# Kernel tuning notes

Measured on AMD Instinct MI355X. Metric: run time of the kernel, lower is better.

Reference implementation:

```python
import jax, jax.numpy as jnp
import numpy as np

N_NODES = 100000
N_EDGES = 800000
D_IN = 128
D_HID = 128
D_OUT = 128
NUM_GRAPHS = 64


def gcn_conv(x, src, dst, W, b, n_nodes):
    """PyG GCNConv: h = D^{-1/2} (A + I) D^{-1/2} (x W) + b, with self-loops included in src/dst."""
    h = x @ W  # [N, d_out]
    deg = jax.ops.segment_sum(jnp.ones_like(dst, dtype=h.dtype), dst, num_segments=n_nodes)
    dinv = jnp.where(deg > 0, jax.lax.rsqrt(deg), 0.0)
    norm = dinv[src] * dinv[dst]  # [E]
    out = jax.ops.segment_sum(h[src] * norm[:, None], dst, num_segments=n_nodes)
    return out + b


def setup_inputs() -> dict:
    key = jax.random.key(0)
    ks = jax.random.split(key, 10)
    x = jax.random.normal(ks[0], (N_NODES, D_IN), dtype=jnp.float32)
    edge_index = jax.random.randint(ks[1], (2, N_EDGES), 0, N_NODES, dtype=jnp.int64)
    batch = jnp.sort(jax.random.randint(ks[2], (N_NODES,), 0, NUM_GRAPHS, dtype=jnp.int64))
    s1 = 1.0 / np.sqrt(D_IN)
    s2 = 1.0 / np.sqrt(D_HID)
    W1 = jax.random.uniform(ks[3], (D_IN, D_HID), jnp.float32, -s1, s1)
    b1 = jnp.zeros((D_HID,), jnp.float32)
    W2 = jax.random.uniform(ks[4], (D_HID, D_HID), jnp.float32, -s2, s2)
    b2 = jnp.zeros((D_HID,), jnp.float32)
    Wfc = jax.random.uniform(ks[5], (D_HID, D_OUT), jnp.float32, -s2, s2)
    bfc = jax.random.uniform(ks[6], (D_OUT,), jnp.float32, -s2, s2)
    return {"x": x, "edge_index": edge_index, "batch": batch,
            "W1": W1, "b1": b1, "W2": W2, "b2": b2, "Wfc": Wfc, "bfc": bfc}


def reference(x, edge_index, batch, W1, b1, W2, b2, Wfc, bfc):
    n = x.shape[0]
    loop = jnp.arange(n, dtype=edge_index.dtype)
    src = jnp.concatenate([edge_index[0], loop])
    dst = jnp.concatenate([edge_index[1], loop])
    h = jax.nn.relu(gcn_conv(x, src, dst, W1, b1, n))
    h = jax.nn.relu(gcn_conv(h, src, dst, W2, b2, n))
    # global_mean_pool over graph ids
    sums = jax.ops.segment_sum(h, batch, num_segments=NUM_GRAPHS)
    cnts = jax.ops.segment_sum(jnp.ones((n,), h.dtype), batch, num_segments=NUM_GRAPHS)
    pooled = sums / jnp.maximum(cnts, 1.0)[:, None]
    return pooled @ Wfc + bfc
```

## Files before the change

kernel.cpp:

```cpp
#include <hip/hip_runtime.h>
#include <hip/hip_bf16.h>

#define N_NODES 100000
#define N_EDGES 800000
#define D 128
#define NG 64
#define SCAN_NB ((N_NODES + 255) / 256)
#define NTILES ((N_NODES + 63) / 64)

typedef __attribute__((ext_vector_type(8))) short short8;
typedef __attribute__((ext_vector_type(4))) float f32x4;
typedef __attribute__((ext_vector_type(2))) float f32x2;

static __device__ __forceinline__ unsigned short f2bf(float f) {
    unsigned u = __float_as_uint(f);
    unsigned r = (u + 0x7FFF + ((u >> 16) & 1)) >> 16;
    return (unsigned short)r;
}
static __device__ __forceinline__ float bf2f(unsigned short b) {
    return __uint_as_float((unsigned)b << 16);
}
static __device__ __forceinline__ unsigned char f2fp8(float v) {
    int p = __builtin_amdgcn_cvt_pk_fp8_f32(v, v, 0, false);
    return (unsigned char)(p & 0xFF);
}


__global__ void hist_kernel(const int* __restrict__ dst, int* __restrict__ deg) {
    int e = blockIdx.x * blockDim.x + threadIdx.x;
    if (e < N_EDGES) atomicAdd(&deg[dst[e]], 1);
}

__global__ __launch_bounds__(256) void scan1_kernel(const int* __restrict__ deg,
                                                    int* __restrict__ rs,
                                                    int* __restrict__ bsum,
                                                    float* __restrict__ dinv) {
    __shared__ int wsum[4];
    int i = blockIdx.x * 256 + threadIdx.x;
    int lane = threadIdx.x & 63;
    int wid = threadIdx.x >> 6;
    int v = (i < N_NODES) ? deg[i] : 0;
    if (i < N_NODES) dinv[i] = rsqrtf((float)v + 1.0f);
    int x = v;
    #pragma unroll
    for (int off = 1; off < 64; off <<= 1) {
        int y = __shfl_up(x, off);
        if (lane >= off) x += y;
    }
    if (lane == 63) wsum[wid] = x;
    __syncthreads();
    int add = 0;
    #pragma unroll
    for (int w = 0; w < 3; ++w) if (w < wid) add += wsum[w];
    int incl = x + add;
    if (i < N_NODES) rs[i] = incl - v;
    if (threadIdx.x == 255) bsum[blockIdx.x] = incl;
}

__global__ __launch_bounds__(512) void scan2_kernel(int* __restrict__ bsum) {
    __shared__ int s[512];
    int t = threadIdx.x;
    int v = (t < SCAN_NB) ? bsum[t] : 0;
    s[t] = v;
    __syncthreads();
    for (int off = 1; off < 512; off <<= 1) {
        int y = (t >= off) ? s[t - off] : 0;
        __syncthreads();
        s[t] += y;
        __syncthreads();
    }
    if (t < SCAN_NB) bsum[t] = s[t] - v;
}

__global__ void scan3_kernel(int* __restrict__ rs, const int* __restrict__ bsum) {
    int i = blockIdx.x * blockDim.x + threadIdx.x;
    if (i < N_NODES) rs[i] += bsum[i >> 8];
    if (i == 0) rs[N_NODES] = N_EDGES;
}

__global__ void fill_kernel(const int* __restrict__ src, const int* __restrict__ dst,
                            const float* __restrict__ dinv, const int* __restrict__ rs,
                            int* __restrict__ cursor, int2* __restrict__ pairs) {
    int e = blockIdx.x * blockDim.x + threadIdx.x;
    if (e < N_EDGES) {
        int d = dst[e];
        int s = src[e];
        int p = rs[d] + atomicAdd(&cursor[d], 1);
        pairs[p] = make_int2(s, __float_as_int(dinv[s] * dinv[d]));
    }
}


__global__ void bounds_kernel(const int* __restrict__ batch, int* __restrict__ start) {
    int g = threadIdx.x;
    if (g > NG) return;
    if (g == NG) { start[NG] = N_NODES; return; }
    int lo = 0, hi = N_NODES;
    while (lo < hi) {
        int mid = (lo + hi) >> 1;
        if (batch[mid] < g) lo = mid + 1; else hi = mid;
    }
    start[g] = lo;
}


template <bool IN_F32>
__global__ __launch_bounds__(512) void xw_mfma_kernel(const void* __restrict__ Xin,
                                                      const float* __restrict__ W,
                                                      unsigned char* __restrict__ Hq) {
    __shared__ __align__(16) unsigned short bt_hi[128 * 128];
    __shared__ __align__(16) unsigned short bt_lo[128 * 128];
    __shared__ __align__(16) unsigned short atile[64 * 128];

    const int t = threadIdx.x;
    const int lane = t & 63;
    const int wid = t >> 6;

    #pragma unroll 4
    for (int i = 0; i < 32; ++i) {
        int idx = t + i * 512;
        int k = idx >> 7;
        int n = idx & 127;
        float w = W[idx];
        unsigned short hi = f2bf(w);
        unsigned short lo = f2bf(w - bf2f(hi));
        int byte = (n * 256 + k * 2) ^ ((n & 7) << 4);
        *(unsigned short*)((char*)bt_hi + byte) = hi;
        *(unsigned short*)((char*)bt_lo + byte) = lo;
    }

    const int mrow = (wid >> 1) * 16;
    const int ncol = (wid & 1) * 64;
    const int ar = mrow + (lane & 15);
    const int ak = (lane >> 4) * 8;

    for (int tile = blockIdx.x; tile < NTILES; tile += gridDim.x) {
        const int node0 = tile * 64;
        __syncthreads();

        #pragma unroll
        for (int p = 0; p < 2; ++p) {
            int j = t + p * 512;
            int row = j >> 4;
            int c8 = (j & 15) * 8;
            int node = node0 + row;
            short8 v = 0;
            if (IN_F32) {
                const float* X = (const float*)Xin;
                if (node < N_NODES) {
                    const float* xr = &X[(size_t)node * 128 + c8];
                    float4 a = *(const float4*)xr;
                    float4 b = *(const float4*)(xr + 4);
                    v[0] = (short)f2bf(a.x); v[1] = (short)f2bf(a.y);
                    v[2] = (short)f2bf(a.z); v[3] = (short)f2bf(a.w);
                    v[4] = (short)f2bf(b.x); v[5] = (short)f2bf(b.y);
                    v[6] = (short)f2bf(b.z); v[7] = (short)f2bf(b.w);
                }
            } else {
                const unsigned short* X = (const unsigned short*)Xin;
                if (node < N_NODES) v = *(const short8*)&X[(size_t)node * 128 + c8];
            }
            int byte = (row * 256 + c8 * 2) ^ ((row & 7) << 4);
            *(short8*)((char*)atile + byte) = v;
        }
        __syncthreads();

        f32x4 acc[4];
        #pragma unroll
        for (int nt = 0; nt < 4; ++nt) acc[nt] = 0.f;

        #pragma unroll
        for (int kc = 0; kc < 128; kc += 32) {
            short8 a = *(const short8*)((const char*)atile +
                        ((ar * 256 + (kc + ak) * 2) ^ ((ar & 7) << 4)));
            #pragma unroll
            for (int nt = 0; nt < 4; ++nt) {
                int col = ncol + nt * 16 + (lane & 15);
                int boff = (col * 256 + (kc + ak) * 2) ^ ((col & 7) << 4);
                short8 bh = *(const short8*)((const char*)bt_hi + boff);
                acc[nt] = __builtin_amdgcn_mfma_f32_16x16x32_bf16(a, bh, acc[nt], 0, 0, 0);
                short8 bl = *(const short8*)((const char*)bt_lo + boff);
                acc[nt] = __builtin_amdgcn_mfma_f32_16x16x32_bf16(a, bl, acc[nt], 0, 0, 0);
            }
        }

        #pragma unroll
        for (int nt = 0; nt < 4; ++nt) {
            #pragma unroll
            for (int r = 0; r < 4; ++r) {
                int node = node0 + mrow + (lane >> 4) * 4 + r;
                if (node < N_NODES)
                    Hq[(size_t)node * 128 + ncol + nt * 16 + (lane & 15)] = f2fp8(acc[nt][r]);
            }
        }
    }
}


#define ACC8(HV, W)                                                        \
    {                                                                      \
        f32x2 _h0 = __builtin_amdgcn_cvt_pk_f32_fp8((int)(HV).x, false);   \
        f32x2 _h1 = __builtin_amdgcn_cvt_pk_f32_fp8((int)(HV).x, true);    \
        f32x2 _h2 = __builtin_amdgcn_cvt_pk_f32_fp8((int)(HV).y, false);   \
        f32x2 _h3 = __builtin_amdgcn_cvt_pk_f32_fp8((int)(HV).y, true);    \
        acc[0] = fmaf(_h0[0], (W), acc[0]); acc[1] = fmaf(_h0[1], (W), acc[1]); \
        acc[2] = fmaf(_h1[0], (W), acc[2]); acc[3] = fmaf(_h1[1], (W), acc[3]); \
        acc[4] = fmaf(_h2[0], (W), acc[4]); acc[5] = fmaf(_h2[1], (W), acc[5]); \
        acc[6] = fmaf(_h3[0], (W), acc[6]); acc[7] = fmaf(_h3[1], (W), acc[7]); \
    }

__global__ __launch_bounds__(256) void gather_kernel(const unsigned char* __restrict__ Hq,
                                                     const int* __restrict__ rs,
                                                     const int2* __restrict__ pairs,
                                                     const float* __restrict__ dinv,
                                                     const float* __restrict__ bias,
                                                     unsigned short* __restrict__ out) {
    int node = blockIdx.x * 4 + (threadIdx.x >> 6);
    if (node >= N_NODES) return;
    const int lane = threadIdx.x & 63;
    const int g = lane >> 4;
    const int fl = lane & 15;

    int beg = rs[node];
    int end = rs[node + 1];
    int deg = end - beg;

    float di = dinv[node];
    float wself = (g == 0) ? di * di : 0.f;

    float acc[8];
    {
        uint2 sv = *(const uint2*)&Hq[(size_t)node * 128 + fl * 8];
        f32x2 a0 = __builtin_amdgcn_cvt_pk_f32_fp8((int)sv.x, false);
        f32x2 a1 = __builtin_amdgcn_cvt_pk_f32_fp8((int)sv.x, true);
        f32x2 a2 = __builtin_amdgcn_cvt_pk_f32_fp8((int)sv.y, false);
        f32x2 a3 = __builtin_amdgcn_cvt_pk_f32_fp8((int)sv.y, true);
        acc[0] = a0[0] * wself; acc[1] = a0[1] * wself;
        acc[2] = a1[0] * wself; acc[3] = a1[1] * wself;
        acc[4] = a2[0] * wself; acc[5] = a2[1] * wself;
        acc[6] = a3[0] * wself; acc[7] = a3[1] * wself;
    }

    if (deg > 0) {
        int2 pall = pairs[beg + min(lane, deg - 1)];
        int niter = (deg + 3) >> 2;

        const int j0 = g, j1 = g + 4, j2 = g + 8, j3 = g + 12;
        int s0 = __shfl(pall.x, j0), s1 = __shfl(pall.x, j1);
        int s2 = __shfl(pall.x, j2), s3 = __shfl(pall.x, j3);
        float w0 = (j0 < deg) ? __int_as_float(__shfl(pall.y, j0)) : 0.f;
        float w1 = (j1 < deg) ? __int_as_float(__shfl(pall.y, j1)) : 0.f;
        float w2 = (j2 < deg) ? __int_as_float(__shfl(pall.y, j2)) : 0.f;
        float w3 = (j3 < deg) ? __int_as_float(__shfl(pall.y, j3)) : 0.f;

        uint2 h0 = make_uint2(0u, 0u), h1 = h0, h2 = h0, h3 = h0;
        h0 = *(const uint2*)&Hq[(size_t)s0 * 128 + fl * 8];
        if (niter > 1) h1 = *(const uint2*)&Hq[(size_t)s1 * 128 + fl * 8];
        if (niter > 2) h2 = *(const uint2*)&Hq[(size_t)s2 * 128 + fl * 8];
        if (niter > 3) h3 = *(const uint2*)&Hq[(size_t)s3 * 128 + fl * 8];

        ACC8(h0, w0);
        ACC8(h1, w1);
        ACC8(h2, w2);
        ACC8(h3, w3);

        if (deg > 16) {
            for (int j = 16 + g; j < deg; j += 4) {
                int2 p = pairs[beg + j];
                float w = __int_as_float(p.y);
                uint2 hv = *(const uint2*)&Hq[(size_t)p.x * 128 + fl * 8];
                ACC8(hv, w);
            }
        }
    }

    #pragma unroll
    for (int mask = 16; mask <= 32; mask <<= 1) {
        #pragma unroll
        for (int j = 0; j < 8; ++j) acc[j] += __shfl_xor(acc[j], mask);
    }

    if (g == 0) {
        float4 bb0 = *(const float4*)&bias[fl * 8];
        float4 bb1 = *(const float4*)&bias[fl * 8 + 4];
        short8 o;
        o[0] = (short)f2bf(fmaxf(acc[0] + bb0.x, 0.f));
        o[1] = (short)f2bf(fmaxf(acc[1] + bb0.y, 0.f));
        o[2] = (short)f2bf(fmaxf(acc[2] + bb0.z, 0.f));
        o[3] = (short)f2bf(fmaxf(acc[3] + bb0.w, 0.f));
        o[4] = (short)f2bf(fmaxf(acc[4] + bb1.x, 0.f));
        o[5] = (short)f2bf(fmaxf(acc[5] + bb1.y, 0.f));
        o[6] = (short)f2bf(fmaxf(acc[6] + bb1.z, 0.f));
        o[7] = (short)f2bf(fmaxf(acc[7] + bb1.w, 0.f));
        *(short8*)&out[(size_t)node * 128 + fl * 8] = o;
    }
}


__global__ __launch_bounds__(256) void pool_kernel(const unsigned short* __restrict__ G,
                                                   const int* __restrict__ start,
                                                   float* __restrict__ sums) {
    __shared__ float red[16][132];
    int g = blockIdx.x >> 4;
    int s = blockIdx.x & 15;
    int n0 = start[g], n1 = start[g + 1];
    int slot = threadIdx.x & 15;
    int nl = threadIdx.x >> 4;

    float acc[8];
    #pragma unroll
    for (int j = 0; j < 8; ++j) acc[j] = 0.f;

    for (int node = n0 + s * 16 + nl; node < n1; node += 256) {
        short8 v = *(const short8*)&G[(size_t)node * 128 + slot * 8];
        #pragma unroll
        for (int j = 0; j < 8; ++j) acc[j] += bf2f((unsigned short)v[j]);
    }

    #pragma unroll
    for (int j = 0; j < 8; ++j) red[nl][slot * 8 + j] = acc[j];
    __syncthreads();
    #pragma unroll
    for (int off = 8; off > 0; off >>= 1) {
        if (nl < off) {
            #pragma unroll
            for (int j = 0; j < 8; ++j)
                red[nl][slot * 8 + j] += red[nl + off][slot * 8 + j];
        }
        __syncthreads();
    }
    if (nl == 0) {
        #pragma unroll
        for (int j = 0; j < 8; ++j)
            unsafeAtomicAdd(&sums[g * D + slot * 8 + j], red[0][slot * 8 + j]);
    }
}


__global__ void fc_kernel(const float* __restrict__ sums, const int* __restrict__ start,
                          const float* __restrict__ Wfc, const float* __restrict__ bfc,
                          float* __restrict__ out) {
    __shared__ __align__(16) float ps[D];
    int g = blockIdx.x;
    int f = threadIdx.x;
    float c = (float)max(start[g + 1] - start[g], 1);
    ps[f] = sums[g * D + f] / c;
    __syncthreads();
    float acc = bfc[f];
    #pragma unroll
    for (int k = 0; k < D; k += 4) {
        float4 pv = *(const float4*)&ps[k];
        acc += pv.x * Wfc[k * D + f] + pv.y * Wfc[(k + 1) * D + f] +
               pv.z * Wfc[(k + 2) * D + f] + pv.w * Wfc[(k + 3) * D + f];
    }
    out[g * D + f] = acc;
}

extern "C" void kernel_launch(void* const* d_in, const int* in_sizes, int n_in,
                              void* d_out, int out_size, void* d_ws, size_t ws_size,
                              hipStream_t stream) {
    const float* x   = (const float*)d_in[0];
    const int* ei    = (const int*)d_in[1];
    const int* batch = (const int*)d_in[2];
    const float* W1  = (const float*)d_in[3];
    const float* b1  = (const float*)d_in[4];
    const float* W2  = (const float*)d_in[5];
    const float* b2  = (const float*)d_in[6];
    const float* Wfc = (const float*)d_in[7];
    const float* bfc = (const float*)d_in[8];
    float* out = (float*)d_out;

    const int* src = ei;
    const int* dst = ei + N_EDGES;

    unsigned char* Hq    = (unsigned char*)d_ws;
    unsigned short* G    = (unsigned short*)(Hq + (size_t)N_NODES * D);
    int2* pairs          = (int2*)(G + (size_t)N_NODES * D);
    float* dinv          = (float*)(pairs + N_EDGES);
    int*   deg           = (int*)(dinv + N_NODES);
    int*   cursor        = deg + N_NODES;
    int*   rs            = cursor + N_NODES;
    int*   bsum          = rs + N_NODES + 4;
    int*   start         = bsum + 512;
    float* sums          = (float*)(start + NG + 8);

    hipMemsetAsync(deg, 0, 2 * N_NODES * sizeof(int), stream);
    hipMemsetAsync(sums, 0, NG * D * sizeof(float), stream);

    hist_kernel<<<(N_EDGES + 255) / 256, 256, 0, stream>>>(dst, deg);
    scan1_kernel<<<SCAN_NB, 256, 0, stream>>>(deg, rs, bsum, dinv);
    scan2_kernel<<<1, 512, 0, stream>>>(bsum);
    scan3_kernel<<<SCAN_NB, 256, 0, stream>>>(rs, bsum);
    fill_kernel<<<(N_EDGES + 255) / 256, 256, 0, stream>>>(src, dst, dinv, rs, cursor, pairs);
    bounds_kernel<<<1, 128, 0, stream>>>(batch, start);

    xw_mfma_kernel<true><<<512, 512, 0, stream>>>(x, W1, Hq);
    gather_kernel<<<(N_NODES + 3) / 4, 256, 0, stream>>>(Hq, rs, pairs, dinv, b1, G);

    xw_mfma_kernel<false><<<512, 512, 0, stream>>>(G, W2, Hq);
    gather_kernel<<<(N_NODES + 3) / 4, 256, 0, stream>>>(Hq, rs, pairs, dinv, b2, G);

    pool_kernel<<<NG * 16, 256, 0, stream>>>(G, start, sums);
    fc_kernel<<<NG, 128, 0, stream>>>(sums, start, Wfc, bfc, out);
}
```

Baseline: 305.7 us.

## Fold symmetric normalization into XW output and drop per-edge weights

The per-edge weight dinv[s]*dinv[d] is factored: H rows are pre-scaled by dinv[src] in the matmul epilogue and the aggregated sum is scaled by dinv[dst] in the gather epilogue. Edge storage shrinks from int2 pairs to plain source ids, and the fill kernel drops the dinv reads. The CSR row-start array now doubles as the cursor through a shifted scan, which removes one array and its memset. Padded lanes point at a zeroed sentinel row instead of using zero weights. This lowers memory traffic in the fill and gather stages, at the cost of rounding dinv-scaled values to fp8.

```diff
diff --git a/kernel.cpp b/kernel.cpp
--- a/kernel.cpp
+++ b/kernel.cpp
@@ -53,7 +53,7 @@
     #pragma unroll
     for (int w = 0; w < 3; ++w) if (w < wid) add += wsum[w];
     int incl = x + add;
-    if (i < N_NODES) rs[i] = incl - v;
+    if (i < N_NODES) rs[i + 1] = incl - v;
     if (threadIdx.x == 255) bsum[blockIdx.x] = incl;
 }
 
@@ -74,25 +74,25 @@
 
 __global__ void scan3_kernel(int* __restrict__ rs, const int* __restrict__ bsum) {
     int i = blockIdx.x * blockDim.x + threadIdx.x;
-    if (i < N_NODES) rs[i] += bsum[i >> 8];
-    if (i == 0) rs[N_NODES] = N_EDGES;
+    if (i < N_NODES) rs[i + 1] += bsum[i >> 8];
+    if (i == 0) rs[0] = 0;
 }
 
 __global__ void fill_kernel(const int* __restrict__ src, const int* __restrict__ dst,
-                            const float* __restrict__ dinv, const int* __restrict__ rs,
-                            int* __restrict__ cursor, int2* __restrict__ pairs) {
+                            int* __restrict__ rs, int* __restrict__ pairs) {
     int e = blockIdx.x * blockDim.x + threadIdx.x;
     if (e < N_EDGES) {
         int d = dst[e];
-        int s = src[e];
-        int p = rs[d] + atomicAdd(&cursor[d], 1);
-        pairs[p] = make_int2(s, __float_as_int(dinv[s] * dinv[d]));
-    }
-}
-
-
-__global__ void bounds_kernel(const int* __restrict__ batch, int* __restrict__ start) {
+        int p = atomicAdd(&rs[1 + d], 1);
+        pairs[p] = src[e];
+    }
+}
+
+
+__global__ void bounds_kernel(const int* __restrict__ batch, int* __restrict__ start,
+                              unsigned int* __restrict__ sentinel) {
     int g = threadIdx.x;
+    if (g < 32) sentinel[g] = 0u;
     if (g > NG) return;
     if (g == NG) { start[NG] = N_NODES; return; }
     int lo = 0, hi = N_NODES;
@@ -107,6 +107,7 @@
 template <bool IN_F32>
 __global__ __launch_bounds__(512) void xw_mfma_kernel(const void* __restrict__ Xin,
                                                       const float* __restrict__ W,
+                                                      const float* __restrict__ dinv,
                                                       unsigned char* __restrict__ Hq) {
     __shared__ __align__(16) unsigned short bt_hi[128 * 128];
     __shared__ __align__(16) unsigned short bt_lo[128 * 128];
@@ -185,33 +186,34 @@
         }
 
         #pragma unroll
-        for (int nt = 0; nt < 4; ++nt) {
-            #pragma unroll
-            for (int r = 0; r < 4; ++r) {
-                int node = node0 + mrow + (lane >> 4) * 4 + r;
-                if (node < N_NODES)
-                    Hq[(size_t)node * 128 + ncol + nt * 16 + (lane & 15)] = f2fp8(acc[nt][r]);
+        for (int r = 0; r < 4; ++r) {
+            int node = node0 + mrow + (lane >> 4) * 4 + r;
+            if (node < N_NODES) {
+                float di = dinv[node];
+                #pragma unroll
+                for (int nt = 0; nt < 4; ++nt)
+                    Hq[(size_t)node * 128 + ncol + nt * 16 + (lane & 15)] = f2fp8(acc[nt][r] * di);
             }
         }
     }
 }
 
 
-#define ACC8(HV, W)                                                        \
+#define ACC8ADD(HV)                                                        \
     {                                                                      \
         f32x2 _h0 = __builtin_amdgcn_cvt_pk_f32_fp8((int)(HV).x, false);   \
         f32x2 _h1 = __builtin_amdgcn_cvt_pk_f32_fp8((int)(HV).x, true);    \
         f32x2 _h2 = __builtin_amdgcn_cvt_pk_f32_fp8((int)(HV).y, false);   \
         f32x2 _h3 = __builtin_amdgcn_cvt_pk_f32_fp8((int)(HV).y, true);    \
-        acc[0] = fmaf(_h0[0], (W), acc[0]); acc[1] = fmaf(_h0[1], (W), acc[1]); \
-        acc[2] = fmaf(_h1[0], (W), acc[2]); acc[3] = fmaf(_h1[1], (W), acc[3]); \
-        acc[4] = fmaf(_h2[0], (W), acc[4]); acc[5] = fmaf(_h2[1], (W), acc[5]); \
-        acc[6] = fmaf(_h3[0], (W), acc[6]); acc[7] = fmaf(_h3[1], (W), acc[7]); \
+        acc[0] += _h0[0]; acc[1] += _h0[1];                                \
+        acc[2] += _h1[0]; acc[3] += _h1[1];                                \
+        acc[4] += _h2[0]; acc[5] += _h2[1];                                \
+        acc[6] += _h3[0]; acc[7] += _h3[1];                                \
     }
 
 __global__ __launch_bounds__(256) void gather_kernel(const unsigned char* __restrict__ Hq,
                                                      const int* __restrict__ rs,
-                                                     const int2* __restrict__ pairs,
+                                                     const int* __restrict__ pairs,
                                                      const float* __restrict__ dinv,
                                                      const float* __restrict__ bias,
                                                      unsigned short* __restrict__ out) {
@@ -225,33 +227,31 @@
     int end = rs[node + 1];
     int deg = end - beg;
 
-    float di = dinv[node];
-    float wself = (g == 0) ? di * di : 0.f;
-
     float acc[8];
-    {
+    if (g == 0) {
         uint2 sv = *(const uint2*)&Hq[(size_t)node * 128 + fl * 8];
         f32x2 a0 = __builtin_amdgcn_cvt_pk_f32_fp8((int)sv.x, false);
         f32x2 a1 = __builtin_amdgcn_cvt_pk_f32_fp8((int)sv.x, true);
         f32x2 a2 = __builtin_amdgcn_cvt_pk_f32_fp8((int)sv.y, false);
         f32x2 a3 = __builtin_amdgcn_cvt_pk_f32_fp8((int)sv.y, true);
-        acc[0] = a0[0] * wself; acc[1] = a0[1] * wself;
-        acc[2] = a1[0] * wself; acc[3] = a1[1] * wself;
-        acc[4] = a2[0] * wself; acc[5] = a2[1] * wself;
-        acc[6] = a3[0] * wself; acc[7] = a3[1] * wself;
+        acc[0] = a0[0]; acc[1] = a0[1];
+        acc[2] = a1[0]; acc[3] = a1[1];
+        acc[4] = a2[0]; acc[5] = a2[1];
+        acc[6] = a3[0]; acc[7] = a3[1];
+    } else {
+        #pragma unroll
+        for (int j = 0; j < 8; ++j) acc[j] = 0.f;
     }
 
     if (deg > 0) {
-        int2 pall = pairs[beg + min(lane, deg - 1)];
+        int pall = pairs[beg + min(lane, deg - 1)];
         int niter = (deg + 3) >> 2;
 
         const int j0 = g, j1 = g + 4, j2 = g + 8, j3 = g + 12;
-        int s0 = __shfl(pall.x, j0), s1 = __shfl(pall.x, j1);
-        int s2 = __shfl(pall.x, j2), s3 = __shfl(pall.x, j3);
-        float w0 = (j0 < deg) ? __int_as_float(__shfl(pall.y, j0)) : 0.f;
-        float w1 = (j1 < deg) ? __int_as_float(__shfl(pall.y, j1)) : 0.f;
-        float w2 = (j2 < deg) ? __int_as_float(__shfl(pall.y, j2)) : 0.f;
-        float w3 = (j3 < deg) ? __int_as_float(__shfl(pall.y, j3)) : 0.f;
+        int s0 = (j0 < deg) ? __shfl(pall, j0) : N_NODES;
+        int s1 = (j1 < deg) ? __shfl(pall, j1) : N_NODES;
+        int s2 = (j2 < deg) ? __shfl(pall, j2) : N_NODES;
+        int s3 = (j3 < deg) ? __shfl(pall, j3) : N_NODES;
 
         uint2 h0 = make_uint2(0u, 0u), h1 = h0, h2 = h0, h3 = h0;
         h0 = *(const uint2*)&Hq[(size_t)s0 * 128 + fl * 8];
@@ -259,17 +259,16 @@
         if (niter > 2) h2 = *(const uint2*)&Hq[(size_t)s2 * 128 + fl * 8];
         if (niter > 3) h3 = *(const uint2*)&Hq[(size_t)s3 * 128 + fl * 8];
 
-        ACC8(h0, w0);
-        ACC8(h1, w1);
-        ACC8(h2, w2);
-        ACC8(h3, w3);
+        ACC8ADD(h0);
+        ACC8ADD(h1);
+        ACC8ADD(h2);
+        ACC8ADD(h3);
 
         if (deg > 16) {
             for (int j = 16 + g; j < deg; j += 4) {
-                int2 p = pairs[beg + j];
-                float w = __int_as_float(p.y);
-                uint2 hv = *(const uint2*)&Hq[(size_t)p.x * 128 + fl * 8];
-                ACC8(hv, w);
+                int s = pairs[beg + j];
+                uint2 hv = *(const uint2*)&Hq[(size_t)s * 128 + fl * 8];
+                ACC8ADD(hv);
             }
         }
     }
@@ -281,17 +280,18 @@
     }
 
     if (g == 0) {
+        float di = dinv[node];
         float4 bb0 = *(const float4*)&bias[fl * 8];
         float4 bb1 = *(const float4*)&bias[fl * 8 + 4];
         short8 o;
-        o[0] = (short)f2bf(fmaxf(acc[0] + bb0.x, 0.f));
-        o[1] = (short)f2bf(fmaxf(acc[1] + bb0.y, 0.f));
-        o[2] = (short)f2bf(fmaxf(acc[2] + bb0.z, 0.f));
-        o[3] = (short)f2bf(fmaxf(acc[3] + bb0.w, 0.f));
-        o[4] = (short)f2bf(fmaxf(acc[4] + bb1.x, 0.f));
-        o[5] = (short)f2bf(fmaxf(acc[5] + bb1.y, 0.f));
-        o[6] = (short)f2bf(fmaxf(acc[6] + bb1.z, 0.f));
-        o[7] = (short)f2bf(fmaxf(acc[7] + bb1.w, 0.f));
+        o[0] = (short)f2bf(fmaxf(fmaf(acc[0], di, bb0.x), 0.f));
+        o[1] = (short)f2bf(fmaxf(fmaf(acc[1], di, bb0.y), 0.f));
+        o[2] = (short)f2bf(fmaxf(fmaf(acc[2], di, bb0.z), 0.f));
+        o[3] = (short)f2bf(fmaxf(fmaf(acc[3], di, bb0.w), 0.f));
+        o[4] = (short)f2bf(fmaxf(fmaf(acc[4], di, bb1.x), 0.f));
+        o[5] = (short)f2bf(fmaxf(fmaf(acc[5], di, bb1.y), 0.f));
+        o[6] = (short)f2bf(fmaxf(fmaf(acc[6], di, bb1.z), 0.f));
+        o[7] = (short)f2bf(fmaxf(fmaf(acc[7], di, bb1.w), 0.f));
         *(short8*)&out[(size_t)node * 128 + fl * 8] = o;
     }
 }
@@ -374,30 +374,30 @@
     const int* dst = ei + N_EDGES;
 
     unsigned char* Hq    = (unsigned char*)d_ws;
-    unsigned short* G    = (unsigned short*)(Hq + (size_t)N_NODES * D);
-    int2* pairs          = (int2*)(G + (size_t)N_NODES * D);
+    unsigned short* G    = (unsigned short*)(Hq + (size_t)(N_NODES + 1) * D);
+    int* pairs           = (int*)(G + (size_t)N_NODES * D);
     float* dinv          = (float*)(pairs + N_EDGES);
     int*   deg           = (int*)(dinv + N_NODES);
-    int*   cursor        = deg + N_NODES;
-    int*   rs            = cursor + N_NODES;
+    int*   rs            = deg + N_NODES;
     int*   bsum          = rs + N_NODES + 4;
     int*   start         = bsum + 512;
     float* sums          = (float*)(start + NG + 8);
 
-    hipMemsetAsync(deg, 0, 2 * N_NODES * sizeof(int), stream);
+    hipMemsetAsync(deg, 0, N_NODES * sizeof(int), stream);
     hipMemsetAsync(sums, 0, NG * D * sizeof(float), stream);
 
     hist_kernel<<<(N_EDGES + 255) / 256, 256, 0, stream>>>(dst, deg);
     scan1_kernel<<<SCAN_NB, 256, 0, stream>>>(deg, rs, bsum, dinv);
     scan2_kernel<<<1, 512, 0, stream>>>(bsum);
     scan3_kernel<<<SCAN_NB, 256, 0, stream>>>(rs, bsum);
-    fill_kernel<<<(N_EDGES + 255) / 256, 256, 0, stream>>>(src, dst, dinv, rs, cursor, pairs);
-    bounds_kernel<<<1, 128, 0, stream>>>(batch, start);
-
-    xw_mfma_kernel<true><<<512, 512, 0, stream>>>(x, W1, Hq);
+    fill_kernel<<<(N_EDGES + 255) / 256, 256, 0, stream>>>(src, dst, rs, pairs);
+    bounds_kernel<<<1, 128, 0, stream>>>(batch, start,
+                                         (unsigned int*)(Hq + (size_t)N_NODES * D));
+
+    xw_mfma_kernel<true><<<512, 512, 0, stream>>>(x, W1, dinv, Hq);
     gather_kernel<<<(N_NODES + 3) / 4, 256, 0, stream>>>(Hq, rs, pairs, dinv, b1, G);
 
-    xw_mfma_kernel<false><<<512, 512, 0, stream>>>(G, W2, Hq);
+    xw_mfma_kernel<false><<<512, 512, 0, stream>>>(G, W2, dinv, Hq);
     gather_kernel<<<(N_NODES + 3) / 4, 256, 0, stream>>>(Hq, rs, pairs, dinv, b2, G);
 
     pool_kernel<<<NG * 16, 256, 0, stream>>>(G, start, sums);
```

New measurement: 314.2 us. 2.8% more time.
